# Kernel optimization log

Hardware: AMD Instinct MI355X
Metric: run time of the kernel (lower is better)

The kernel has to match this reference:

```python
import jax, jax.numpy as jnp
import numpy as np

H = 256                      # latent_channels = LSTM hidden
OC = [32, 64, 64, 128]       # out_channels per mesh level
V = [5023, 1256, 314, 79, 20]  # vertex counts per level (fine -> coarse)
L = 9                        # spiral length
T = 64                       # audio frames (batch for decoder)


def setup_inputs() -> dict:
    key = jax.random.key(0)
    ks = iter(jax.random.split(key, 80))
    f32 = jnp.float32

    def nrm(shape, fan_in):
        return jax.random.normal(next(ks), shape, f32) * (1.0 / np.sqrt(fan_in))

    inp = {}
    inp['audio'] = jax.random.normal(next(ks), (T, 768), f32)
    inp['actor'] = jax.random.normal(next(ks), (V[0], 3), f32)

    # 5-layer bidirectional LSTM; layer 0 input 768, layers 1-4 input 2H
    inp['lstm_Wih0'] = nrm((2, 4 * H, 768), 768)
    inp['lstm_Whh0'] = nrm((2, 4 * H, H), H)
    inp['lstm_b0'] = jnp.zeros((2, 4 * H), f32)
    inp['lstm_Wih'] = nrm((4, 2, 4 * H, 2 * H), 2 * H)
    inp['lstm_Whh'] = nrm((4, 2, 4 * H, H), H)
    inp['lstm_b'] = jnp.zeros((4, 2, 4 * H), f32)

    # decoder entry fc: 2*latent -> num_vert * oc[-1]
    inp['fc_W'] = nrm((V[4] * OC[3], 2 * H), 2 * H)
    inp['fc_b'] = jnp.zeros((V[4] * OC[3],), f32)

    # SpiralConv weights (torch Linear layout: [out, in*L])
    inp['conv3_W'] = nrm((128, 128 * L), 128 * L); inp['conv3_b'] = jnp.zeros((128,), f32)
    inp['conv2_W'] = nrm((64, 128 * L), 128 * L);  inp['conv2_b'] = jnp.zeros((64,), f32)
    inp['conv1_W'] = nrm((64, 64 * L), 64 * L);    inp['conv1_b'] = jnp.zeros((64,), f32)
    inp['conv0_W'] = nrm((32, 64 * L), 64 * L);    inp['conv0_b'] = jnp.zeros((32,), f32)
    inp['head_W'] = nrm((3, 32 * L), 32 * L);      inp['head_b'] = jnp.zeros((3,), f32)

    # spiral indices per level: [V_j, L] with values in [0, V_j)
    for j in range(4):
        inp[f'idx{j}'] = jax.random.randint(next(ks), (V[j], L), 0, V[j], jnp.int32)

    # up_transform[j] sparse [V_j, V_{j+1}], ~3 nnz per row (COO)
    for j in range(4):
        nnz = 3 * V[j]
        inp[f'rows{j}'] = jnp.repeat(jnp.arange(V[j], dtype=jnp.int32), 3)
        inp[f'cols{j}'] = jax.random.randint(next(ks), (nnz,), 0, V[j + 1], jnp.int32)
        inp[f'vals{j}'] = jax.random.uniform(next(ks), (nnz,), f32) / 3.0
    return inp


def _lstm_dir(x, Wih, Whh, b, reverse):
    # x: [T, Din]; torch gate order i, f, g, o
    def step(carry, xt):
        h, c = carry
        g = Wih @ xt + Whh @ h + b            # [4H]
        i, f, gg, o = jnp.split(g, 4)
        c = jax.nn.sigmoid(f) * c + jax.nn.sigmoid(i) * jnp.tanh(gg)
        h = jax.nn.sigmoid(o) * jnp.tanh(c)
        return (h, c), h
    init = (jnp.zeros((H,), x.dtype), jnp.zeros((H,), x.dtype))
    _, hs = jax.lax.scan(step, init, x, reverse=reverse)
    return hs  # [T, H], aligned with input order


def _bilstm(x, Wih, Whh, b):
    hf = _lstm_dir(x, Wih[0], Whh[0], b[0], False)
    hb = _lstm_dir(x, Wih[1], Whh[1], b[1], True)
    return jnp.concatenate([hf, hb], axis=-1)  # [T, 2H]


def _pool(x, rows, cols, vals, n_out):
    # sparse up-transform: out[t, r] = sum_nnz vals * x[t, cols]
    g = x[:, cols, :] * vals[None, :, None]                       # [T, nnz, C]
    return jax.ops.segment_sum(g.swapaxes(0, 1), rows, num_segments=n_out).swapaxes(0, 1)


def _spiral(x, idx, W, b):
    # gather fixed spiral neighborhoods then dense linear
    g = x[:, idx, :].reshape(x.shape[0], idx.shape[0], -1)        # [T, V, L*C]
    return g @ W.T + b


def reference(audio, actor, lstm_Wih0, lstm_Whh0, lstm_b0, lstm_Wih, lstm_Whh, lstm_b,
              fc_W, fc_b, conv3_W, conv3_b, conv2_W, conv2_b, conv1_W, conv1_b,
              conv0_W, conv0_b, head_W, head_b,
              vals3, vals2, vals1, vals0,
              idx0, idx1, idx2, idx3,
              rows3, cols3, rows2, cols2, rows1, cols1, rows0, cols0):
    # audio embedding: 5-layer bidirectional LSTM (batch = 1)
    z = _bilstm(audio, lstm_Wih0, lstm_Whh0, lstm_b0)
    for l in range(4):
        z = _bilstm(z, lstm_Wih[l], lstm_Whh[l], lstm_b[l])       # [T, 2H]

    # decode
    x = (z @ fc_W.T + fc_b).reshape(z.shape[0], V[4], OC[3])      # [T, 20, 128]
    x = jax.nn.elu(_spiral(_pool(x, rows3, cols3, vals3, V[3]), idx3, conv3_W, conv3_b))
    x = jax.nn.elu(_spiral(_pool(x, rows2, cols2, vals2, V[2]), idx2, conv2_W, conv2_b))
    x = jax.nn.elu(_spiral(_pool(x, rows1, cols1, vals1, V[1]), idx1, conv1_W, conv1_b))
    x = jax.nn.elu(_spiral(_pool(x, rows0, cols0, vals0, V[0]), idx0, conv0_W, conv0_b))
    x = _spiral(x, idx0, head_W, head_b)                          # [T, 5023, 3]
    return x + actor[None]
```

## Files before the change

kernel.cpp:

```cpp
#include <hip/hip_runtime.h>
#include <hip/hip_bf16.h>

typedef __attribute__((ext_vector_type(8))) __bf16 bf16x8;
typedef __attribute__((ext_vector_type(4))) float  f32x4;
typedef __attribute__((ext_vector_type(4))) int    i32x4;

#define SCOPE_AGENT __HIP_MEMORY_SCOPE_AGENT

static __device__ __forceinline__ f32x4 mfma16(bf16x8 a, bf16x8 b, f32x4 c) {
    return __builtin_amdgcn_mfma_f32_16x16x32_bf16(a, b, c, 0, 0, 0);
}
static __device__ __forceinline__ i32x4 mfma_i8(i32x4 a, i32x4 b, i32x4 c) {
    return __builtin_amdgcn_mfma_i32_16x16x64_i8(a, b, c, 0, 0, 0);
}
static __device__ __forceinline__ float sigm(float x)  { return 1.0f / (1.0f + __expf(-x)); }
static __device__ __forceinline__ float tanh_(float x) { return 1.0f - 2.0f / (__expf(2.0f * x) + 1.0f); }

static __device__ __forceinline__ bf16x8 cvt8(const float* __restrict__ p) {
    const float4* q = (const float4*)p;
    float4 a = q[0], b = q[1];
    bf16x8 r;
    r[0] = (__bf16)a.x; r[1] = (__bf16)a.y; r[2] = (__bf16)a.z; r[3] = (__bf16)a.w;
    r[4] = (__bf16)b.x; r[5] = (__bf16)b.y; r[6] = (__bf16)b.z; r[7] = (__bf16)b.w;
    return r;
}
static __device__ __forceinline__ void signal_add(unsigned int* p) {
    __hip_atomic_fetch_add(p, 1u, __ATOMIC_RELEASE, SCOPE_AGENT);
}
template <int SLP>
static __device__ __forceinline__ void wait_eq(unsigned int* p, unsigned int v) {
    while (__hip_atomic_load(p, __ATOMIC_RELAXED, SCOPE_AGENT) != v)
        __builtin_amdgcn_s_sleep(SLP);
    (void)__hip_atomic_load(p, __ATOMIC_ACQUIRE, SCOPE_AGENT);
}
union g4u { unsigned long long q; __bf16 h[4]; };

#define ZBUF_OFF   1024
#define GX_OFF     132096
#define CONVW_OFF  66560
#define ARENA_A    621248
#define ARENA_B    21195456
#define WHHQ_BOFF  11534336
#define SWP_BOFF   14155776

#define NB_LSTM 18
#define NB_WHH  1280
#define NB_FCW  640

__global__ __launch_bounds__(512) __attribute__((amdgpu_waves_per_eu(2, 2)))
void lstm_fused(
    const float* __restrict__ audio,
    const float* __restrict__ Wih0,
    const float* __restrict__ WihL,
    const float* __restrict__ Whh0, const float* __restrict__ WhhL,
    signed char* __restrict__ WhhQ, float* __restrict__ swp,
    const float* __restrict__ b0, const float* __restrict__ bL,
    const float* __restrict__ fcW, __bf16* __restrict__ fcWb,
    unsigned short* __restrict__ Gx_g,
    unsigned int* __restrict__ flags,
    unsigned short* __restrict__ zbuf)
{
    const int bid = blockIdx.x;
    const int tid = threadIdx.x;
    const int wave = tid >> 6, lane = tid & 63, ln = lane & 15, quad = lane >> 4;

    __shared__ __align__(16) signed char    hq[2][256];
    __shared__ __align__(16) unsigned short gx_l[16384];

    if (bid >= NB_LSTM) {
        if (bid < NB_LSTM + NB_WHH) {
            const int g  = (bid - NB_LSTM) * 8 + wave;
            const int dl = g >> 10;
            const int r  = g & 1023;
            const float* src = (dl < 2 ? Whh0 + (size_t)dl * 262144
                                       : WhhL + (size_t)(dl - 2) * 262144) + (size_t)r * 256;
            float4 v = *(const float4*)(src + lane * 4);
            float am = fmaxf(fmaxf(fabsf(v.x), fabsf(v.y)), fmaxf(fabsf(v.z), fabsf(v.w)));
            #pragma unroll
            for (int m = 1; m < 64; m <<= 1) am = fmaxf(am, __shfl_xor(am, m));
            const float inv = am > 0.f ? 127.f / am : 0.f;
            int q0 = __float2int_rn(v.x * inv), q1 = __float2int_rn(v.y * inv);
            int q2 = __float2int_rn(v.z * inv), q3 = __float2int_rn(v.w * inv);
            unsigned pk = (q0 & 255) | ((q1 & 255) << 8) | ((q2 & 255) << 16) | ((q3 & 255) << 24);
            const int gate = r >> 8, cell = r & 255;
            const int m  = cell * 4 + gate;
            const int lm = m & 15, mt = m >> 4;
            const int k  = lane * 4;
            const int kc = k >> 6, qd = (k >> 4) & 3, j = k & 15;
            size_t addr = ((((size_t)dl * 64 + mt) * 4 + kc) * 64 + (qd * 16 + lm)) * 16 + j;
            *(unsigned*)(WhhQ + addr) = pk;
            if (lane == 0) swp[(size_t)dl * 1024 + cell * 4 + gate] = am / 127.f;
            __syncthreads();
            if (tid == 0) { __threadfence(); signal_add(&flags[60]); }
        } else {
            int f = ((bid - NB_LSTM - NB_WHH) * 512 + tid) * 4;
            if (f < 1310720) {
                float4 v = *(const float4*)(fcW + f);
                g4u u;
                u.h[0] = (__bf16)v.x; u.h[1] = (__bf16)v.y;
                u.h[2] = (__bf16)v.z; u.h[3] = (__bf16)v.w;
                *(unsigned long long*)(fcWb + f) = u.q;
            }
        }
        return;
    }

    if (bid < 16) {
        const int dir = bid >> 3, sub = bid & 7;
        const int gmt = sub * 8 + wave;
        const int m_a = gmt * 16 + ln;
        const int r_a = (m_a & 3) * 256 + (m_a >> 2);
        unsigned short* GxO = Gx_g + (size_t)dir * 65536;

        {
            const float* Wih_l = Wih0 + (size_t)dir * 786432;
            const float* b_l   = b0 + (size_t)dir * 1024;
            bf16x8 afr[24];
            #pragma unroll
            for (int kc = 0; kc < 24; ++kc)
                afr[kc] = cvt8(Wih_l + (size_t)r_a * 768 + kc * 32 + quad * 8);
            float bv[4];
            #pragma unroll
            for (int reg = 0; reg < 4; ++reg) {
                const int m_row = gmt * 16 + quad * 4 + reg;
                bv[reg] = b_l[(m_row & 3) * 256 + (m_row >> 2)];
            }
            for (int ii = 0; ii < 4; ++ii) {
                const int nt = dir ? 3 - ii : ii;
                const int t  = nt * 16 + ln;
                f32x4 acA = (f32x4){0.f, 0.f, 0.f, 0.f};
                f32x4 acB = (f32x4){0.f, 0.f, 0.f, 0.f};
                #pragma unroll
                for (int kc = 0; kc < 24; kc += 2) {
                    acA = mfma16(afr[kc],
                                 cvt8(audio + (size_t)t * 768 + kc * 32 + quad * 8), acA);
                    acB = mfma16(afr[kc + 1],
                                 cvt8(audio + (size_t)t * 768 + (kc + 1) * 32 + quad * 8), acB);
                }
                f32x4 acc = acA + acB;
                #pragma unroll
                for (int reg = 0; reg < 4; ++reg) {
                    const int m_row = gmt * 16 + quad * 4 + reg;
                    __bf16 v = (__bf16)(acc[reg] + bv[reg]);
                    GxO[(size_t)t * 1024 + m_row] = __builtin_bit_cast(unsigned short, v);
                }
                __syncthreads();
                if (tid == 0) { __threadfence(); signal_add(&flags[(0 * 2 + dir) * 4 + nt]); }
            }
        }

        for (int l = 1; l < 5; ++l) {
            const float* Wih_l = WihL + (size_t)((l - 1) * 2 + dir) * 524288;
            const float* b_l   = bL + (size_t)((l - 1) * 2 + dir) * 1024;
            bf16x8 afr[16];
            #pragma unroll
            for (int kc = 0; kc < 16; ++kc)
                afr[kc] = cvt8(Wih_l + (size_t)r_a * 512 + kc * 32 + quad * 8);
            float bv[4];
            #pragma unroll
            for (int reg = 0; reg < 4; ++reg) {
                const int m_row = gmt * 16 + quad * 4 + reg;
                bv[reg] = b_l[(m_row & 3) * 256 + (m_row >> 2)];
            }
            if (tid == 0) wait_eq<4>(&flags[48 + (l - 1)], 2u);
            __syncthreads();
            const __bf16* zp = (const __bf16*)(zbuf + (size_t)((l - 1) & 1) * 32768);

            for (int ii = 0; ii < 4; ++ii) {
                const int nt = dir ? 3 - ii : ii;
                const int t  = nt * 16 + ln;
                f32x4 acA = (f32x4){0.f, 0.f, 0.f, 0.f};
                f32x4 acB = (f32x4){0.f, 0.f, 0.f, 0.f};
                #pragma unroll
                for (int kc = 0; kc < 16; kc += 2) {
                    acA = mfma16(afr[kc],
                                 *(const bf16x8*)(zp + (size_t)t * 512 + kc * 32 + quad * 8), acA);
                    acB = mfma16(afr[kc + 1],
                                 *(const bf16x8*)(zp + (size_t)t * 512 + (kc + 1) * 32 + quad * 8), acB);
                }
                f32x4 acc = acA + acB;
                #pragma unroll
                for (int reg = 0; reg < 4; ++reg) {
                    const int m_row = gmt * 16 + quad * 4 + reg;
                    __bf16 v = (__bf16)(acc[reg] + bv[reg]);
                    GxO[(size_t)t * 1024 + m_row] = __builtin_bit_cast(unsigned short, v);
                }
                __syncthreads();
                if (tid == 0) { __threadfence(); signal_add(&flags[(l * 2 + dir) * 4 + nt]); }
            }
        }
    } else {
        const int dir = bid - 16;
        const unsigned short* Gx_d = Gx_g + (size_t)dir * 65536;
        const bool owner = (ln < 8);
        const int cell = wave * 32 + ln * 4 + quad;
        const int gcell = owner ? cell : 0;
        const i32x4 czero = (i32x4){0, 0, 0, 0};

        if (tid == 0) wait_eq<4>(&flags[60], (unsigned)NB_WHH);
        __syncthreads();

        for (int l = 0; l < 5; ++l) {
            const int dl = l * 2 + dir;
            i32x4 wf[8][4];
            const i32x4* wb = (const i32x4*)(WhhQ + (size_t)dl * 262144);
            #pragma unroll
            for (int i = 0; i < 8; ++i)
                #pragma unroll
                for (int kc = 0; kc < 4; ++kc)
                    wf[i][kc] = wb[(size_t)(((wave * 8 + i) * 4 + kc)) * 64 + lane];
            float sc0 = 0.f, sc1 = 0.f, sc2 = 0.f, sc3 = 0.f;
            if (owner) {
                float4 s4 = *(const float4*)(swp + (size_t)dl * 1024 + cell * 4);
                const float f = 1.f / 127.f;
                sc0 = s4.x * f; sc1 = s4.y * f; sc2 = s4.z * f; sc3 = s4.w * f;
            }
            if (tid < 64) ((unsigned int*)hq[0])[tid] = 0;
            float cst = 0.f;
            unsigned short* zl = zbuf + (size_t)(l & 1) * 32768;
            const int gxbase = (l * 2 + dir) * 4;

            for (int s = 0; s < 64; ++s) {
                if ((s & 15) == 0) {
                    const int nt = dir ? 3 - (s >> 4) : (s >> 4);
                    if (tid == 0) wait_eq<1>(&flags[gxbase + nt], 8u);
                    __syncthreads();
                    const float4* src = (const float4*)(Gx_d + (size_t)nt * 16384);
                    float4* dst = (float4*)gx_l;
                    #pragma unroll
                    for (int i = 0; i < 4; ++i) dst[i * 512 + tid] = src[i * 512 + tid];
                    __syncthreads();
                }
                const int t = dir ? (63 - s) : s;
                const int tl = t & 15;
                const int cur = s & 1, nxt = cur ^ 1;
                g4u gx;
                gx.q = *(const unsigned long long*)&gx_l[tl * 1024 + gcell * 4];
                i32x4 acc[8];
                {
                    i32x4 b0v = *(const i32x4*)&hq[cur][quad * 16];
                    #pragma unroll
                    for (int i = 0; i < 8; ++i) acc[i] = mfma_i8(wf[i][0], b0v, czero);
                }
                #pragma unroll
                for (int kc = 1; kc < 4; ++kc) {
                    i32x4 b = *(const i32x4*)&hq[cur][kc * 64 + quad * 16];
                    #pragma unroll
                    for (int i = 0; i < 8; ++i) acc[i] = mfma_i8(wf[i][kc], b, acc[i]);
                }
                i32x4 a = acc[0];
                #pragma unroll
                for (int j = 1; j < 8; ++j) if (ln == j) a = acc[j];
                if (owner) {
                    float gi = (float)a[0] * sc0 + (float)gx.h[0];
                    float gf = (float)a[1] * sc1 + (float)gx.h[1];
                    float gg = (float)a[2] * sc2 + (float)gx.h[2];
                    float go = (float)a[3] * sc3 + (float)gx.h[3];
                    cst = sigm(gf) * cst + sigm(gi) * tanh_(gg);
                    float h = sigm(go) * tanh_(cst);
                    int q = __float2int_rn(h * 127.f);
                    hq[nxt][cell] = (signed char)q;
                    __bf16 zv = (__bf16)((float)q * (1.f / 127.f));
                    zl[(size_t)t * 512 + dir * 256 + cell] =
                        __builtin_bit_cast(unsigned short, zv);
                }
                __syncthreads();
            }
            if (tid == 0) { __threadfence(); signal_add(&flags[48 + l]); }
        }
    }
}

__global__ __launch_bounds__(256) void fc_kernel(
    const __bf16* __restrict__ zb, const __bf16* __restrict__ W,
    const float* __restrict__ bb, __bf16* __restrict__ out,
    const float* __restrict__ c3W, const float* __restrict__ c2W,
    const float* __restrict__ c1W, const float* __restrict__ c0W,
    const float* __restrict__ hW, __bf16* __restrict__ convWb)
{
    const int tid = threadIdx.x;
    if (blockIdx.x >= 40) {
        int f = ((blockIdx.x - 40) * 256 + tid) * 4;
        if (f < 277344) {
            const float* src; int off;
            if (f < 147456)      { src = c3W; off = f; }
            else if (f < 221184) { src = c2W; off = f - 147456; }
            else if (f < 258048) { src = c1W; off = f - 221184; }
            else if (f < 276480) { src = c0W; off = f - 258048; }
            else                 { src = hW;  off = f - 276480; }
            float4 v = *(const float4*)(src + off);
            g4u u;
            u.h[0] = (__bf16)v.x; u.h[1] = (__bf16)v.y;
            u.h[2] = (__bf16)v.z; u.h[3] = (__bf16)v.w;
            *(unsigned long long*)(convWb + f) = u.q;
        }
        return;
    }
    const int wave = tid >> 6, lane = tid & 63, ln = lane & 15, quad = lane >> 4;
    const int nbase = blockIdx.x * 64;
    f32x4 acc[4];
    #pragma unroll
    for (int nt = 0; nt < 4; nt++) acc[nt] = (f32x4){0.f, 0.f, 0.f, 0.f};
    #pragma unroll 2
    for (int kc = 0; kc < 16; kc++) {
        const int k0 = kc * 32 + quad * 8;
        bf16x8 a = *(const bf16x8*)(zb + (size_t)(wave * 16 + ln) * 512 + k0);
        #pragma unroll
        for (int nt = 0; nt < 4; nt++) {
            bf16x8 b = *(const bf16x8*)(W + (size_t)(nbase + nt * 16 + ln) * 512 + k0);
            acc[nt] = mfma16(a, b, acc[nt]);
        }
    }
    #pragma unroll
    for (int nt = 0; nt < 4; nt++) {
        const int n = nbase + nt * 16 + ln;
        const float bv = bb[n];
        #pragma unroll
        for (int reg = 0; reg < 4; reg++) {
            const int t = wave * 16 + quad * 4 + reg;
            out[(size_t)((n >> 7) * 64 + t) * 128 + (n & 127)] = (__bf16)(acc[nt][reg] + bv);
        }
    }
}

template <int C>
__global__ __launch_bounds__(256) void pool_kernel(
    const __bf16* __restrict__ in, __bf16* __restrict__ out,
    const int* __restrict__ cols, const float* __restrict__ vals, int V)
{
    const int P = 64 * C / 8;
    const int gid = blockIdx.x * 256 + threadIdx.x;
    if (gid >= V * P) return;
    const int r = gid / P;
    const int rem = gid - r * P;
    float acc[8] = {0.f, 0.f, 0.f, 0.f, 0.f, 0.f, 0.f, 0.f};
    #pragma unroll
    for (int s = 0; s < 3; s++) {
        const int col = cols[3 * r + s];
        const float vv = vals[3 * r + s];
        bf16x8 x = *(const bf16x8*)(in + (size_t)col * 64 * C + rem * 8);
        #pragma unroll
        for (int e = 0; e < 8; e++) acc[e] += vv * (float)x[e];
    }
    bf16x8 ov;
    #pragma unroll
    for (int e = 0; e < 8; e++) ov[e] = (__bf16)acc[e];
    *(bf16x8*)(out + (size_t)r * 64 * C + rem * 8) = ov;
}

template <int CIN, int COUT>
__global__ __launch_bounds__(64) void conv_kernel(
    const __bf16* __restrict__ in, __bf16* __restrict__ out,
    const int* __restrict__ idx, const __bf16* __restrict__ W,
    const float* __restrict__ bias)
{
    constexpr int K = 9 * CIN;
    constexpr int NT = COUT / 16;
    constexpr int NKC = K / 32;
    const int v = blockIdx.x;
    const int lane = threadIdx.x, ln = lane & 15, quad = lane >> 4;
    const int t0 = blockIdx.y * 16;
    __shared__ int sIdx[9];
    if (lane < 9) sIdx[lane] = idx[v * 9 + lane];
    __syncthreads();
    f32x4 acc[NT];
    #pragma unroll
    for (int nt = 0; nt < NT; nt++) acc[nt] = (f32x4){0.f, 0.f, 0.f, 0.f};
    const int tt = t0 + ln;
    for (int kc = 0; kc < NKC; kc++) {
        const int k0 = kc * 32;
        const int l = k0 / CIN;
        const int c = (k0 & (CIN - 1)) + quad * 8;
        const int row = sIdx[l];
        bf16x8 a = *(const bf16x8*)(in + ((size_t)row * 64 + tt) * CIN + c);
        #pragma unroll
        for (int nt = 0; nt < NT; nt++) {
            bf16x8 b = *(const bf16x8*)(W + (size_t)(nt * 16 + ln) * K + k0 + quad * 8);
            acc[nt] = mfma16(a, b, acc[nt]);
        }
    }
    #pragma unroll
    for (int nt = 0; nt < NT; nt++) {
        const int n = nt * 16 + ln;
        const float bv = bias[n];
        #pragma unroll
        for (int reg = 0; reg < 4; reg++) {
            const int t = t0 + quad * 4 + reg;
            float val = acc[nt][reg] + bv;
            val = val > 0.f ? val : (__expf(val) - 1.f);
            out[((size_t)v * 64 + t) * COUT + n] = (__bf16)val;
        }
    }
}

__global__ __launch_bounds__(64) void head_kernel(
    const __bf16* __restrict__ in, float* __restrict__ out,
    const int* __restrict__ idx, const __bf16* __restrict__ W,
    const float* __restrict__ bias, const float* __restrict__ actor)
{
    const int v = blockIdx.x;
    const int lane = threadIdx.x, ln = lane & 15, quad = lane >> 4;
    const int t0 = blockIdx.y * 16;
    __shared__ int sIdx[9];
    if (lane < 9) sIdx[lane] = idx[v * 9 + lane];
    __syncthreads();
    f32x4 acc = (f32x4){0.f, 0.f, 0.f, 0.f};
    const int tt = t0 + ln;
    const int rown = ln < 3 ? ln : 0;
    #pragma unroll
    for (int kc = 0; kc < 9; kc++) {
        const int row = sIdx[kc];
        bf16x8 a = *(const bf16x8*)(in + ((size_t)row * 64 + tt) * 32 + quad * 8);
        bf16x8 b = *(const bf16x8*)(W + (size_t)rown * 288 + kc * 32 + quad * 8);
        acc = mfma16(a, b, acc);
    }
    if (ln < 3) {
        const float bv = bias[ln];
        const float av = actor[v * 3 + ln];
        #pragma unroll
        for (int reg = 0; reg < 4; reg++) {
            const int t = t0 + quad * 4 + reg;
            out[((size_t)t * 5023 + v) * 3 + ln] = acc[reg] + bv + av;
        }
    }
}

extern "C" void kernel_launch(void* const* d_in, const int* in_sizes, int n_in,
                              void* d_out, int out_size, void* d_ws, size_t ws_size,
                              hipStream_t stream) {
    const float* audio = (const float*)d_in[0];
    const float* actor = (const float*)d_in[1];
    const float* Wih0  = (const float*)d_in[2];
    const float* Whh0  = (const float*)d_in[3];
    const float* b0    = (const float*)d_in[4];
    const float* WihL  = (const float*)d_in[5];
    const float* WhhL  = (const float*)d_in[6];
    const float* bLs   = (const float*)d_in[7];
    const float* fcW   = (const float*)d_in[8];
    const float* fcb   = (const float*)d_in[9];
    const float* c3W = (const float*)d_in[10]; const float* c3b = (const float*)d_in[11];
    const float* c2W = (const float*)d_in[12]; const float* c2b = (const float*)d_in[13];
    const float* c1W = (const float*)d_in[14]; const float* c1b = (const float*)d_in[15];
    const float* c0W = (const float*)d_in[16]; const float* c0b = (const float*)d_in[17];
    const float* hW  = (const float*)d_in[18]; const float* hb  = (const float*)d_in[19];
    const int* idx0 = (const int*)d_in[20];
    const int* idx1 = (const int*)d_in[21];
    const int* idx2 = (const int*)d_in[22];
    const int* idx3 = (const int*)d_in[23];
    const int* cols0 = (const int*)d_in[25]; const float* vals0 = (const float*)d_in[26];
    const int* cols1 = (const int*)d_in[28]; const float* vals1 = (const float*)d_in[29];
    const int* cols2 = (const int*)d_in[31]; const float* vals2 = (const float*)d_in[32];
    const int* cols3 = (const int*)d_in[34]; const float* vals3 = (const float*)d_in[35];

    char* ws = (char*)d_ws;
    unsigned int*   flags = (unsigned int*)ws;
    unsigned short* zbuf  = (unsigned short*)(ws + ZBUF_OFF);
    unsigned short* GxG   = (unsigned short*)(ws + GX_OFF);
    __bf16*         convWb = (__bf16*)(ws + CONVW_OFF);
    char* arenaA = ws + ARENA_A;
    char* arenaB = ws + ARENA_B;

    signed char* whhq = (signed char*)(arenaB + WHHQ_BOFF);
    float*       swp  = (float*)(arenaB + SWP_BOFF);
    __bf16*      fcWb = (__bf16*)(arenaB + 2097152);

    __bf16* x4b = (__bf16*)arenaA;
    __bf16* p3  = (__bf16*)arenaB;
    __bf16* c3o = (__bf16*)arenaA;
    __bf16* p2  = (__bf16*)arenaB;
    __bf16* c2o = (__bf16*)arenaA;
    __bf16* p1  = (__bf16*)arenaB;
    __bf16* c1o = (__bf16*)arenaA;
    __bf16* p0  = (__bf16*)arenaB;
    __bf16* c0o = (__bf16*)arenaA;

    (void)hipMemsetAsync(ws, 0, 1024, stream);

    lstm_fused<<<NB_LSTM + NB_WHH + NB_FCW, 512, 0, stream>>>(
        audio, Wih0, WihL, Whh0, WhhL, whhq, swp, b0, bLs,
        fcW, fcWb, GxG, flags, zbuf);

    fc_kernel<<<40 + 271, 256, 0, stream>>>((const __bf16*)zbuf, fcWb, fcb, x4b,
                                            c3W, c2W, c1W, c0W, hW, convWb);

    { int n = 79 * 64 * 128 / 8;
      pool_kernel<128><<<(n + 255) / 256, 256, 0, stream>>>(x4b, p3, cols3, vals3, 79);
      conv_kernel<128, 128><<<dim3(79, 4), 64, 0, stream>>>(p3, c3o, idx3, convWb + 0, c3b); }
    { int n = 314 * 64 * 128 / 8;
      pool_kernel<128><<<(n + 255) / 256, 256, 0, stream>>>(c3o, p2, cols2, vals2, 314);
      conv_kernel<128, 64><<<dim3(314, 4), 64, 0, stream>>>(p2, c2o, idx2, convWb + 147456, c2b); }
    { int n = 1256 * 64 * 64 / 8;
      pool_kernel<64><<<(n + 255) / 256, 256, 0, stream>>>(c2o, p1, cols1, vals1, 1256);
      conv_kernel<64, 64><<<dim3(1256, 4), 64, 0, stream>>>(p1, c1o, idx1, convWb + 221184, c1b); }
    { int n = 5023 * 64 * 64 / 8;
      pool_kernel<64><<<(n + 255) / 256, 256, 0, stream>>>(c1o, p0, cols0, vals0, 5023);
      conv_kernel<64, 32><<<dim3(5023, 4), 64, 0, stream>>>(p0, c0o, idx0, convWb + 258048, c0b); }

    head_kernel<<<dim3(5023, 4), 64, 0, stream>>>(c0o, (float*)d_out, idx0,
                                                  convWb + 276480, hb, actor);
}
```

Baseline: 866.7 us.

## Split weight pre-conversion into separate kernel and batch LSTM z writes per block

Moves the int8 quantisation of Whh and the bf16 conversion of fc_W out of the fused LSTM launch into a standalone precvt kernel that runs before it. The LSTM recurrent blocks no longer spin on a completion flag for the conversion blocks. The main loop is restructured into 4 blocks of 16 steps. Hidden states for each block are staged as int8 in shared memory and written to the global z buffer as coalesced bf16 after the block, instead of a scattered 2-byte store every step. The trade-off is an extra launch and serialised conversion, where the conversion previously overlapped with the Gx projection.

Result: faster. 818.3 us (median of 2 runs) (-5.6%).

```diff
diff --git a/kernel.cpp b/kernel.cpp
--- a/kernel.cpp
+++ b/kernel.cpp
@@ -43,19 +43,54 @@
 #define WHHQ_BOFF  11534336
 #define SWP_BOFF   14155776
 
-#define NB_LSTM 18
-#define NB_WHH  1280
-#define NB_FCW  640
+__global__ __launch_bounds__(256) void precvt(
+    const float* __restrict__ Whh0, const float* __restrict__ WhhL,
+    signed char* __restrict__ WhhQ, float* __restrict__ swp,
+    const float* __restrict__ fcW, __bf16* __restrict__ fcWb)
+{
+    if (blockIdx.x >= 2560) {
+        int f = ((blockIdx.x - 2560) * 256 + threadIdx.x) * 4;
+        if (f < 1310720) {
+            float4 v = *(const float4*)(fcW + f);
+            g4u u;
+            u.h[0] = (__bf16)v.x; u.h[1] = (__bf16)v.y;
+            u.h[2] = (__bf16)v.z; u.h[3] = (__bf16)v.w;
+            *(unsigned long long*)(fcWb + f) = u.q;
+        }
+        return;
+    }
+    const int g  = blockIdx.x * 4 + (threadIdx.x >> 6);
+    const int dl = g >> 10;
+    const int r  = g & 1023;
+    const int lane = threadIdx.x & 63;
+    const float* src = (dl < 2 ? Whh0 + (size_t)dl * 262144
+                               : WhhL + (size_t)(dl - 2) * 262144) + (size_t)r * 256;
+    float4 v = *(const float4*)(src + lane * 4);
+    float am = fmaxf(fmaxf(fabsf(v.x), fabsf(v.y)), fmaxf(fabsf(v.z), fabsf(v.w)));
+    #pragma unroll
+    for (int m = 1; m < 64; m <<= 1) am = fmaxf(am, __shfl_xor(am, m));
+    const float inv = am > 0.f ? 127.f / am : 0.f;
+    int q0 = __float2int_rn(v.x * inv), q1 = __float2int_rn(v.y * inv);
+    int q2 = __float2int_rn(v.z * inv), q3 = __float2int_rn(v.w * inv);
+    unsigned pk = (q0 & 255) | ((q1 & 255) << 8) | ((q2 & 255) << 16) | ((q3 & 255) << 24);
+    const int gate = r >> 8, cell = r & 255;
+    const int m  = cell * 4 + gate;
+    const int lm = m & 15, mt = m >> 4;
+    const int k  = lane * 4;
+    const int kc = k >> 6, qd = (k >> 4) & 3, j = k & 15;
+    size_t addr = ((((size_t)dl * 64 + mt) * 4 + kc) * 64 + (qd * 16 + lm)) * 16 + j;
+    *(unsigned*)(WhhQ + addr) = pk;
+    if (lane == 0) swp[(size_t)dl * 1024 + cell * 4 + gate] = am / 127.f;
+}
 
 __global__ __launch_bounds__(512) __attribute__((amdgpu_waves_per_eu(2, 2)))
 void lstm_fused(
     const float* __restrict__ audio,
     const float* __restrict__ Wih0,
     const float* __restrict__ WihL,
-    const float* __restrict__ Whh0, const float* __restrict__ WhhL,
-    signed char* __restrict__ WhhQ, float* __restrict__ swp,
+    const signed char* __restrict__ WhhQ,
+    const float* __restrict__ swp,
     const float* __restrict__ b0, const float* __restrict__ bL,
-    const float* __restrict__ fcW, __bf16* __restrict__ fcWb,
     unsigned short* __restrict__ Gx_g,
     unsigned int* __restrict__ flags,
     unsigned short* __restrict__ zbuf)
@@ -65,45 +100,8 @@
     const int wave = tid >> 6, lane = tid & 63, ln = lane & 15, quad = lane >> 4;
 
     __shared__ __align__(16) signed char    hq[2][256];
+    __shared__ __align__(16) signed char    zq[4096];
     __shared__ __align__(16) unsigned short gx_l[16384];
-
-    if (bid >= NB_LSTM) {
-        if (bid < NB_LSTM + NB_WHH) {
-            const int g  = (bid - NB_LSTM) * 8 + wave;
-            const int dl = g >> 10;
-            const int r  = g & 1023;
-            const float* src = (dl < 2 ? Whh0 + (size_t)dl * 262144
-                                       : WhhL + (size_t)(dl - 2) * 262144) + (size_t)r * 256;
-            float4 v = *(const float4*)(src + lane * 4);
-            float am = fmaxf(fmaxf(fabsf(v.x), fabsf(v.y)), fmaxf(fabsf(v.z), fabsf(v.w)));
-            #pragma unroll
-            for (int m = 1; m < 64; m <<= 1) am = fmaxf(am, __shfl_xor(am, m));
-            const float inv = am > 0.f ? 127.f / am : 0.f;
-            int q0 = __float2int_rn(v.x * inv), q1 = __float2int_rn(v.y * inv);
-            int q2 = __float2int_rn(v.z * inv), q3 = __float2int_rn(v.w * inv);
-            unsigned pk = (q0 & 255) | ((q1 & 255) << 8) | ((q2 & 255) << 16) | ((q3 & 255) << 24);
-            const int gate = r >> 8, cell = r & 255;
-            const int m  = cell * 4 + gate;
-            const int lm = m & 15, mt = m >> 4;
-            const int k  = lane * 4;
-            const int kc = k >> 6, qd = (k >> 4) & 3, j = k & 15;
-            size_t addr = ((((size_t)dl * 64 + mt) * 4 + kc) * 64 + (qd * 16 + lm)) * 16 + j;
-            *(unsigned*)(WhhQ + addr) = pk;
-            if (lane == 0) swp[(size_t)dl * 1024 + cell * 4 + gate] = am / 127.f;
-            __syncthreads();
-            if (tid == 0) { __threadfence(); signal_add(&flags[60]); }
-        } else {
-            int f = ((bid - NB_LSTM - NB_WHH) * 512 + tid) * 4;
-            if (f < 1310720) {
-                float4 v = *(const float4*)(fcW + f);
-                g4u u;
-                u.h[0] = (__bf16)v.x; u.h[1] = (__bf16)v.y;
-                u.h[2] = (__bf16)v.z; u.h[3] = (__bf16)v.w;
-                *(unsigned long long*)(fcWb + f) = u.q;
-            }
-        }
-        return;
-    }
 
     if (bid < 16) {
         const int dir = bid >> 3, sub = bid & 7;
@@ -197,9 +195,6 @@
         const int gcell = owner ? cell : 0;
         const i32x4 czero = (i32x4){0, 0, 0, 0};
 
-        if (tid == 0) wait_eq<4>(&flags[60], (unsigned)NB_WHH);
-        __syncthreads();
-
         for (int l = 0; l < 5; ++l) {
             const int dl = l * 2 + dir;
             i32x4 wf[8][4];
@@ -220,51 +215,65 @@
             unsigned short* zl = zbuf + (size_t)(l & 1) * 32768;
             const int gxbase = (l * 2 + dir) * 4;
 
-            for (int s = 0; s < 64; ++s) {
-                if ((s & 15) == 0) {
-                    const int nt = dir ? 3 - (s >> 4) : (s >> 4);
-                    if (tid == 0) wait_eq<1>(&flags[gxbase + nt], 8u);
-                    __syncthreads();
+            for (int blk = 0; blk < 4; ++blk) {
+                const int nt = dir ? 3 - blk : blk;
+                if (tid == 0) wait_eq<1>(&flags[gxbase + nt], 8u);
+                __syncthreads();
+                {
                     const float4* src = (const float4*)(Gx_d + (size_t)nt * 16384);
                     float4* dst = (float4*)gx_l;
                     #pragma unroll
                     for (int i = 0; i < 4; ++i) dst[i * 512 + tid] = src[i * 512 + tid];
+                }
+                __syncthreads();
+
+                for (int ss = 0; ss < 16; ++ss) {
+                    const int s = blk * 16 + ss;
+                    const int tl = dir ? 15 - ss : ss;
+                    const int cur = s & 1, nxt = cur ^ 1;
+                    g4u gx;
+                    gx.q = *(const unsigned long long*)&gx_l[tl * 1024 + gcell * 4];
+                    i32x4 acc[8];
+                    {
+                        i32x4 b0v = *(const i32x4*)&hq[cur][quad * 16];
+                        #pragma unroll
+                        for (int i = 0; i < 8; ++i) acc[i] = mfma_i8(wf[i][0], b0v, czero);
+                    }
+                    #pragma unroll
+                    for (int kc = 1; kc < 4; ++kc) {
+                        i32x4 b = *(const i32x4*)&hq[cur][kc * 64 + quad * 16];
+                        #pragma unroll
+                        for (int i = 0; i < 8; ++i) acc[i] = mfma_i8(wf[i][kc], b, acc[i]);
+                    }
+                    i32x4 a = acc[0];
+                    #pragma unroll
+                    for (int j = 1; j < 8; ++j) if (ln == j) a = acc[j];
+                    if (owner) {
+                        float gi = (float)a[0] * sc0 + (float)gx.h[0];
+                        float gf = (float)a[1] * sc1 + (float)gx.h[1];
+                        float gg = (float)a[2] * sc2 + (float)gx.h[2];
+                        float go = (float)a[3] * sc3 + (float)gx.h[3];
+                        cst = sigm(gf) * cst + sigm(gi) * tanh_(gg);
+                        float h = sigm(go) * tanh_(cst);
+                        int q = __float2int_rn(h * 127.f);
+                        hq[nxt][cell] = (signed char)q;
+                        zq[tl * 256 + cell] = (signed char)q;
+                    }
                     __syncthreads();
                 }
-                const int t = dir ? (63 - s) : s;
-                const int tl = t & 15;
-                const int cur = s & 1, nxt = cur ^ 1;
-                g4u gx;
-                gx.q = *(const unsigned long long*)&gx_l[tl * 1024 + gcell * 4];
-                i32x4 acc[8];
-                {
-                    i32x4 b0v = *(const i32x4*)&hq[cur][quad * 16];
+                #pragma unroll
+                for (int i = 0; i < 2; ++i) {
+                    const int d = i * 512 + tid;
+                    const int tf = d >> 4, cb = (d & 15) * 4;
+                    unsigned u = ((const unsigned*)zq)[d];
+                    g4u o;
                     #pragma unroll
-                    for (int i = 0; i < 8; ++i) acc[i] = mfma_i8(wf[i][0], b0v, czero);
-                }
-                #pragma unroll
-                for (int kc = 1; kc < 4; ++kc) {
-                    i32x4 b = *(const i32x4*)&hq[cur][kc * 64 + quad * 16];
-                    #pragma unroll
-                    for (int i = 0; i < 8; ++i) acc[i] = mfma_i8(wf[i][kc], b, acc[i]);
-                }
-                i32x4 a = acc[0];
-                #pragma unroll
-                for (int j = 1; j < 8; ++j) if (ln == j) a = acc[j];
-                if (owner) {
-                    float gi = (float)a[0] * sc0 + (float)gx.h[0];
-                    float gf = (float)a[1] * sc1 + (float)gx.h[1];
-                    float gg = (float)a[2] * sc2 + (float)gx.h[2];
-                    float go = (float)a[3] * sc3 + (float)gx.h[3];
-                    cst = sigm(gf) * cst + sigm(gi) * tanh_(gg);
-                    float h = sigm(go) * tanh_(cst);
-                    int q = __float2int_rn(h * 127.f);
-                    hq[nxt][cell] = (signed char)q;
-                    __bf16 zv = (__bf16)((float)q * (1.f / 127.f));
-                    zl[(size_t)t * 512 + dir * 256 + cell] =
-                        __builtin_bit_cast(unsigned short, zv);
-                }
-                __syncthreads();
+                    for (int j = 0; j < 4; ++j) {
+                        int bch = (int)(signed char)(u >> (8 * j));
+                        o.h[j] = (__bf16)((float)bch * (1.f / 127.f));
+                    }
+                    *(unsigned long long*)(zl + (size_t)(nt * 16 + tf) * 512 + dir * 256 + cb) = o.q;
+                }
             }
             if (tid == 0) { __threadfence(); signal_add(&flags[48 + l]); }
         }
@@ -476,9 +485,10 @@
 
     (void)hipMemsetAsync(ws, 0, 1024, stream);
 
-    lstm_fused<<<NB_LSTM + NB_WHH + NB_FCW, 512, 0, stream>>>(
-        audio, Wih0, WihL, Whh0, WhhL, whhq, swp, b0, bLs,
-        fcW, fcWb, GxG, flags, zbuf);
+    precvt<<<3840, 256, 0, stream>>>(Whh0, WhhL, whhq, swp, fcW, fcWb);
+
+    lstm_fused<<<18, 512, 0, stream>>>(audio, Wih0, WihL, whhq, swp, b0, bLs,
+                                       GxG, flags, zbuf);
 
     fc_kernel<<<40 + 271, 256, 0, stream>>>((const __bf16*)zbuf, fcWb, fcb, x4b,
                                             c3W, c2W, c1W, c0W, hW, convWb);
```
